# Kernel optimization log

Hardware: AMD Instinct MI355X
Metric: run time of the kernel (lower is better)

## Reference

```python
import jax, jax.numpy as jnp
import numpy as np

DIM = 1024
NUM_HEADS = 16
HEAD_DIM = DIM // NUM_HEADS
SCALE = HEAD_DIM ** -0.5
B, N = 2, 2048


def setup_inputs() -> dict:
    key = jax.random.key(0)
    k_x, k_qkv, k_prjw, k_prjb = jax.random.split(key, 4)
    # nn.Linear(dim, 3*dim, bias=False): weight [3*dim, dim]
    s = 1.0 / np.sqrt(DIM)
    return {
        "x": jax.random.normal(k_x, (B, N, DIM), dtype=jnp.float32),
        "w_qkv": jax.random.uniform(k_qkv, (3 * DIM, DIM), jnp.float32, -s, s),
        "w_prj": jax.random.uniform(k_prjw, (DIM, DIM), jnp.float32, -s, s),
        "b_prj": jax.random.uniform(k_prjb, (DIM,), jnp.float32, -s, s),
    }


def reference(x, w_qkv, w_prj, b_prj):
    Bb, Nn, C = x.shape
    qkv = jnp.einsum("bnc,dc->bnd", x, w_qkv)            # [B,N,3C]
    qkv = qkv.reshape(Bb, Nn, 3, NUM_HEADS, HEAD_DIM)
    qkv = jnp.transpose(qkv, (2, 0, 3, 1, 4))            # [3,B,H,N,hd]
    q, k, v = qkv[0], qkv[1], qkv[2]
    attn = jnp.einsum("bhqd,bhkd->bhqk", q, k) * SCALE   # [B,H,N,N]
    attn = jax.nn.softmax(attn, axis=-1)
    out = jnp.einsum("bhqk,bhkd->bhqd", attn, v)         # [B,H,N,hd]
    out = jnp.transpose(out, (0, 2, 1, 3)).reshape(Bb, Nn, C)
    # dropout layers are identity at eval / p=0
    return jnp.einsum("bnc,dc->bnd", out, w_prj) + b_prj
```

## Files before the change

kernel.cpp:

```cpp
#include <hip/hip_runtime.h>

typedef unsigned short u16;
typedef unsigned int u32;
typedef __attribute__((ext_vector_type(8))) short s16x8;
typedef __attribute__((ext_vector_type(4))) float f32x4;

#define DIM    1024
#define NHEADS 16
#define HD     64
#define NSEQ   2048
#define QKVN   3072

__device__ __forceinline__ u16 f2bf(float f) {
  u32 u = __float_as_uint(f);
  u += 0x7FFF + ((u >> 16) & 1);
  return (u16)(u >> 16);
}

__device__ __forceinline__ float vexp2(float x) {
  float r;
  asm volatile("v_exp_f32 %0, %1" : "=v"(r) : "v"(x));
  return r;
}

__device__ __forceinline__ void async16(const u16* g, u16* l) {
  __builtin_amdgcn_global_load_lds(
      (const __attribute__((address_space(1))) unsigned int*)g,
      (__attribute__((address_space(3))) unsigned int*)l, 16, 0, 0);
}

__global__ void cast_all(const float* __restrict__ x, const float* __restrict__ wq,
                         const float* __restrict__ wp, u16* __restrict__ xo,
                         u16* __restrict__ wqo, u16* __restrict__ wpo) {
  int i = blockIdx.x * 256 + threadIdx.x;
  const float4* src; u16* dst; int off;
  if (i < 1048576)      { src = (const float4*)x;  dst = xo;  off = i; }
  else if (i < 1835008) { src = (const float4*)wq; dst = wqo; off = i - 1048576; }
  else                  { src = (const float4*)wp; dst = wpo; off = i - 1835008; }
  float4 f = src[off];
  ushort4 o;
  o.x = f2bf(f.x); o.y = f2bf(f.y); o.z = f2bf(f.z); o.w = f2bf(f.w);
  ((ushort4*)dst)[off] = o;
}

template <bool FINAL>
__global__ __launch_bounds__(256, 3) void gemm_bt(
    const u16* __restrict__ A, const u16* __restrict__ Bw, u16* __restrict__ qkv,
    u16* __restrict__ vt, const float* __restrict__ bias, float* __restrict__ outp) {
  constexpr int K = 1024;
  constexpr int BM = FINAL ? 64 : 128;
  constexpr int MT = FINAL ? 64 : 32;
  constexpr int IT = FINAL ? 2 : 4;
  constexpr int ACALLS = BM / 8;
  constexpr int TCALLS = ACALLS + 16;
  constexpr int PW = TCALLS / 4;
  const int bm = blockIdx.x % MT;
  const int bn = blockIdx.x / MT;
  const int tid = threadIdx.x;
  const int wave = tid >> 6, lane = tid & 63;
  const int q4 = lane >> 4, l15 = lane & 15;
  const int wm = wave >> 1, wn = wave & 1;
  const int m0 = bm * BM, n0 = bn * 128;

  __shared__ alignas(16) u16 lsA[BM * 64];
  __shared__ alignas(16) u16 lsB[128 * 64];

  f32x4 acc[IT][4];
#pragma unroll
  for (int i = 0; i < IT; i++)
#pragma unroll
    for (int j = 0; j < 4; j++) acc[i][j] = (f32x4){0.f, 0.f, 0.f, 0.f};

  for (int k0 = 0; k0 < K; k0 += 64) {
    __syncthreads();
#pragma unroll
    for (int j = 0; j < PW; ++j) {
      int t = wave * PW + j;
      if (t < ACALLS) {
        int lin = t * 64 + lane;
        int r = lin >> 3, cs = lin & 7, c = cs ^ (r & 7);
        async16(A + (size_t)(m0 + r) * K + k0 + c * 8, lsA + t * 512);
      } else {
        int tb = t - ACALLS;
        int lin = tb * 64 + lane;
        int r = lin >> 3, cs = lin & 7, c = cs ^ (r & 7);
        async16(Bw + (size_t)(n0 + r) * K + k0 + c * 8, lsB + tb * 512);
      }
    }
    __syncthreads();
#pragma unroll
    for (int kc = 0; kc < 2; ++kc) {
      s16x8 af[IT], bfr[4];
#pragma unroll
      for (int i = 0; i < IT; ++i) {
        int r = wm * (IT * 16) + i * 16 + l15;
        int c = (kc * 4 + q4) ^ (r & 7);
        af[i] = *(const s16x8*)(lsA + r * 64 + c * 8);
      }
#pragma unroll
      for (int j = 0; j < 4; ++j) {
        int r = wn * 64 + j * 16 + l15;
        int c = (kc * 4 + q4) ^ (r & 7);
        bfr[j] = *(const s16x8*)(lsB + r * 64 + c * 8);
      }
#pragma unroll
      for (int i = 0; i < IT; ++i)
#pragma unroll
        for (int j = 0; j < 4; ++j)
          acc[i][j] = __builtin_amdgcn_mfma_f32_16x16x32_bf16(af[i], bfr[j], acc[i][j], 0, 0, 0);
    }
  }

#pragma unroll
  for (int i = 0; i < IT; i++) {
#pragma unroll
    for (int j = 0; j < 4; j++) {
      int n = n0 + wn * 64 + j * 16 + l15;
      int mb = m0 + wm * (IT * 16) + i * 16 + q4 * 4;
      if (FINAL) {
#pragma unroll
        for (int r = 0; r < 4; r++)
          outp[(size_t)(mb + r) * DIM + n] = acc[i][j][r] + bias[n];
      } else if (n < 2048) {
#pragma unroll
        for (int r = 0; r < 4; r++)
          qkv[(size_t)(mb + r) * QKVN + n] = f2bf(acc[i][j][r]);
      } else {
        int b = mb >> 11, tok = mb & 2047;
        int h = (n >> 6) & 15, hd = n & 63;
        ushort4 pk;
        pk.x = f2bf(acc[i][j][0]); pk.y = f2bf(acc[i][j][1]);
        pk.z = f2bf(acc[i][j][2]); pk.w = f2bf(acc[i][j][3]);
        *(ushort4*)(vt + ((size_t)((b * NHEADS + h) * HD + hd)) * NSEQ + tok) = pk;
      }
    }
  }
}

__global__ __launch_bounds__(256, 2) void attn_kernel(const u16* __restrict__ qkv,
                                                      const u16* __restrict__ vt,
                                                      u16* __restrict__ aout) {
  const int blk = blockIdx.x;
  const int bh = blk & 31, qt = blk >> 5;
  const int b = bh >> 4, h = bh & 15;
  const int tid = threadIdx.x;
  const int wave = tid >> 6, lane = tid & 63;
  const int q4 = lane >> 4, l15 = lane & 15;

  __shared__ alignas(16) u16 lsK[2][64 * 64];
  __shared__ alignas(16) u16 lsV[2][64 * 64];
  __shared__ alignas(16) u16 lsP[4][16 * 72];

  const float QSCALE = 0.18033688011112042f;
  s16x8 aq[2][2];
#pragma unroll
  for (int rt = 0; rt < 2; ++rt)
#pragma unroll
    for (int kc = 0; kc < 2; ++kc) {
      int row = b * NSEQ + qt * 128 + wave * 32 + rt * 16 + l15;
      uint4 d = *(const uint4*)(qkv + (size_t)row * QKVN + h * HD + kc * 32 + q4 * 8);
      u32 w[4] = {d.x, d.y, d.z, d.w};
      s16x8 f;
#pragma unroll
      for (int j = 0; j < 8; ++j) {
        u16 u = (u16)(w[j >> 1] >> ((j & 1) * 16));
        float v = __uint_as_float(((u32)u) << 16) * QSCALE;
        f[j] = (short)f2bf(v);
      }
      aq[rt][kc] = f;
    }

  f32x4 o[2][4];
  float lsum[2][4] = {{0.f, 0.f, 0.f, 0.f}, {0.f, 0.f, 0.f, 0.f}};
#pragma unroll
  for (int rt = 0; rt < 2; ++rt)
#pragma unroll
    for (int ht = 0; ht < 4; ++ht) o[rt][ht] = (f32x4){0.f, 0.f, 0.f, 0.f};

  auto stage = [&](int kt, int buf) {
#pragma unroll
    for (int j = 0; j < 2; ++j) {
      int t = wave * 2 + j;
      int lin = t * 64 + lane;
      int r = lin >> 3, c = (lin & 7) ^ (r & 7);
      async16(qkv + (size_t)(b * NSEQ + kt * 64 + r) * QKVN + DIM + h * HD + c * 8,
              lsK[buf] + t * 512);
      async16(vt + (size_t)(bh * HD + r) * NSEQ + kt * 64 + c * 8,
              lsV[buf] + t * 512);
    }
  };

  stage(0, 0);

  for (int kt = 0; kt < 32; ++kt) {
    const int buf = kt & 1;
    __syncthreads();
    if (kt + 1 < 32) stage(kt + 1, buf ^ 1);

#pragma unroll
    for (int rt = 0; rt < 2; ++rt) {
      f32x4 s[4];
#pragma unroll
      for (int ct = 0; ct < 4; ++ct) s[ct] = (f32x4){0.f, 0.f, 0.f, 0.f};
#pragma unroll
      for (int kc = 0; kc < 2; ++kc) {
#pragma unroll
        for (int ct = 0; ct < 4; ++ct) {
          int r = ct * 16 + l15;
          int c = (kc * 4 + q4) ^ (r & 7);
          s16x8 bk = *(const s16x8*)(lsK[buf] + r * 64 + c * 8);
          s[ct] = __builtin_amdgcn_mfma_f32_16x16x32_bf16(aq[rt][kc], bk, s[ct], 0, 0, 0);
        }
      }

#pragma unroll
      for (int ct = 0; ct < 4; ++ct)
#pragma unroll
        for (int r = 0; r < 4; ++r) {
          u32 u = __float_as_uint(vexp2(s[ct][r]));
          lsum[rt][r] += __uint_as_float(u & 0xffff0000u);
          lsP[wave][(q4 * 4 + r) * 72 + ct * 16 + l15] = (u16)(u >> 16);
        }

#pragma unroll
      for (int kc = 0; kc < 2; ++kc) {
        s16x8 pa = *(const s16x8*)(lsP[wave] + l15 * 72 + kc * 32 + q4 * 8);
#pragma unroll
        for (int ht = 0; ht < 4; ++ht) {
          int r = ht * 16 + l15;
          int c = (kc * 4 + q4) ^ (r & 7);
          s16x8 vb = *(const s16x8*)(lsV[buf] + r * 64 + c * 8);
          o[rt][ht] = __builtin_amdgcn_mfma_f32_16x16x32_bf16(pa, vb, o[rt][ht], 0, 0, 0);
        }
      }
    }
  }

#pragma unroll
  for (int off = 1; off < 16; off <<= 1)
#pragma unroll
    for (int rt = 0; rt < 2; ++rt)
#pragma unroll
      for (int r = 0; r < 4; ++r) lsum[rt][r] += __shfl_xor(lsum[rt][r], off, 64);

#pragma unroll
  for (int rt = 0; rt < 2; ++rt) {
    float inv[4];
#pragma unroll
    for (int r = 0; r < 4; ++r) inv[r] = 1.0f / lsum[rt][r];
#pragma unroll
    for (int ht = 0; ht < 4; ++ht)
#pragma unroll
      for (int r = 0; r < 4; ++r) {
        int n = qt * 128 + wave * 32 + rt * 16 + q4 * 4 + r;
        int col = h * HD + ht * 16 + l15;
        aout[(size_t)(b * NSEQ + n) * DIM + col] = f2bf(o[rt][ht][r] * inv[r]);
      }
  }
}

extern "C" void kernel_launch(void* const* d_in, const int* in_sizes, int n_in,
                              void* d_out, int out_size, void* d_ws, size_t ws_size,
                              hipStream_t stream) {
  const float* x     = (const float*)d_in[0];
  const float* w_qkv = (const float*)d_in[1];
  const float* w_prj = (const float*)d_in[2];
  const float* b_prj = (const float*)d_in[3];
  float* out = (float*)d_out;

  char* ws = (char*)d_ws;
  u16* x_bf    = (u16*)(ws);
  u16* wqkv_bf = (u16*)(ws + (size_t)(8u << 20));
  u16* wprj_bf = (u16*)(ws + (size_t)(14u << 20));
  u16* qkv     = (u16*)(ws + (size_t)(16u << 20));
  u16* vt      = (u16*)(ws + (size_t)(40u << 20));
  u16* aout    = (u16*)(ws + (size_t)(48u << 20));

  cast_all<<<8192, 256, 0, stream>>>(x, w_qkv, w_prj, x_bf, wqkv_bf, wprj_bf);
  gemm_bt<false><<<32 * 24, 256, 0, stream>>>(x_bf, wqkv_bf, qkv, vt, nullptr, nullptr);
  attn_kernel<<<512, 256, 0, stream>>>(qkv, vt, aout);
  gemm_bt<true><<<64 * 8, 256, 0, stream>>>(aout, wprj_bf, nullptr, nullptr, b_prj, out);
}
```

Measured before the change: 189.4 us.

## Keep softmax P in registers via transposed QK^T and shrink GEMM K-tile

New measurement: 188.0 us. No clear change (-0.7%).

```diff
diff --git a/kernel.cpp b/kernel.cpp
--- a/kernel.cpp
+++ b/kernel.cpp
@@ -3,6 +3,7 @@
 typedef unsigned short u16;
 typedef unsigned int u32;
 typedef __attribute__((ext_vector_type(8))) short s16x8;
+typedef __attribute__((ext_vector_type(4))) short s16x4;
 typedef __attribute__((ext_vector_type(4))) float f32x4;
 
 #define DIM    1024
@@ -51,8 +52,8 @@
   constexpr int BM = FINAL ? 64 : 128;
   constexpr int MT = FINAL ? 64 : 32;
   constexpr int IT = FINAL ? 2 : 4;
-  constexpr int ACALLS = BM / 8;
-  constexpr int TCALLS = ACALLS + 16;
+  constexpr int ACALLS = BM / 16;
+  constexpr int TCALLS = ACALLS + 8;
   constexpr int PW = TCALLS / 4;
   const int bm = blockIdx.x % MT;
   const int bn = blockIdx.x / MT;
@@ -62,8 +63,8 @@
   const int wm = wave >> 1, wn = wave & 1;
   const int m0 = bm * BM, n0 = bn * 128;
 
-  __shared__ alignas(16) u16 lsA[BM * 64];
-  __shared__ alignas(16) u16 lsB[128 * 64];
+  __shared__ alignas(16) u16 lsA[BM * 32];
+  __shared__ alignas(16) u16 lsB[128 * 32];
 
   f32x4 acc[IT][4];
 #pragma unroll
@@ -71,44 +72,35 @@
 #pragma unroll
     for (int j = 0; j < 4; j++) acc[i][j] = (f32x4){0.f, 0.f, 0.f, 0.f};
 
-  for (int k0 = 0; k0 < K; k0 += 64) {
+  for (int k0 = 0; k0 < K; k0 += 32) {
     __syncthreads();
 #pragma unroll
     for (int j = 0; j < PW; ++j) {
       int t = wave * PW + j;
       if (t < ACALLS) {
         int lin = t * 64 + lane;
-        int r = lin >> 3, cs = lin & 7, c = cs ^ (r & 7);
+        int r = lin >> 2, c = lin & 3;
         async16(A + (size_t)(m0 + r) * K + k0 + c * 8, lsA + t * 512);
       } else {
         int tb = t - ACALLS;
         int lin = tb * 64 + lane;
-        int r = lin >> 3, cs = lin & 7, c = cs ^ (r & 7);
+        int r = lin >> 2, c = lin & 3;
         async16(Bw + (size_t)(n0 + r) * K + k0 + c * 8, lsB + tb * 512);
       }
     }
     __syncthreads();
-#pragma unroll
-    for (int kc = 0; kc < 2; ++kc) {
-      s16x8 af[IT], bfr[4];
-#pragma unroll
-      for (int i = 0; i < IT; ++i) {
-        int r = wm * (IT * 16) + i * 16 + l15;
-        int c = (kc * 4 + q4) ^ (r & 7);
-        af[i] = *(const s16x8*)(lsA + r * 64 + c * 8);
-      }
-#pragma unroll
-      for (int j = 0; j < 4; ++j) {
-        int r = wn * 64 + j * 16 + l15;
-        int c = (kc * 4 + q4) ^ (r & 7);
-        bfr[j] = *(const s16x8*)(lsB + r * 64 + c * 8);
-      }
-#pragma unroll
-      for (int i = 0; i < IT; ++i)
-#pragma unroll
-        for (int j = 0; j < 4; ++j)
-          acc[i][j] = __builtin_amdgcn_mfma_f32_16x16x32_bf16(af[i], bfr[j], acc[i][j], 0, 0, 0);
-    }
+    s16x8 af[IT], bfr[4];
+#pragma unroll
+    for (int i = 0; i < IT; ++i)
+      af[i] = *(const s16x8*)(lsA + (wm * (IT * 16) + i * 16 + l15) * 32 + q4 * 8);
+#pragma unroll
+    for (int j = 0; j < 4; ++j)
+      bfr[j] = *(const s16x8*)(lsB + (wn * 64 + j * 16 + l15) * 32 + q4 * 8);
+#pragma unroll
+    for (int i = 0; i < IT; ++i)
+#pragma unroll
+      for (int j = 0; j < 4; ++j)
+        acc[i][j] = __builtin_amdgcn_mfma_f32_16x16x32_bf16(af[i], bfr[j], acc[i][j], 0, 0, 0);
   }
 
 #pragma unroll
@@ -149,7 +141,6 @@
 
   __shared__ alignas(16) u16 lsK[2][64 * 64];
   __shared__ alignas(16) u16 lsV[2][64 * 64];
-  __shared__ alignas(16) u16 lsP[4][16 * 72];
 
   const float QSCALE = 0.18033688011112042f;
   s16x8 aq[2][2];
@@ -171,7 +162,7 @@
     }
 
   f32x4 o[2][4];
-  float lsum[2][4] = {{0.f, 0.f, 0.f, 0.f}, {0.f, 0.f, 0.f, 0.f}};
+  float lsum[2] = {0.f, 0.f};
 #pragma unroll
   for (int rt = 0; rt < 2; ++rt)
 #pragma unroll
@@ -197,57 +188,71 @@
     __syncthreads();
     if (kt + 1 < 32) stage(kt + 1, buf ^ 1);
 
+    s16x8 kf[2][4];
+#pragma unroll
+    for (int kc = 0; kc < 2; ++kc)
+#pragma unroll
+      for (int ct = 0; ct < 4; ++ct) {
+        int r = ct * 16 + l15;
+        int c = (kc * 4 + q4) ^ (r & 7);
+        kf[kc][ct] = *(const s16x8*)(lsK[buf] + r * 64 + c * 8);
+      }
+    s16x4 vf[4][4];
+#pragma unroll
+    for (int ct = 0; ct < 4; ++ct)
+#pragma unroll
+      for (int ht = 0; ht < 4; ++ht) {
+        int row = ht * 16 + l15;
+        int g = ct * 2 + (q4 >> 1);
+        int p = g ^ (row & 7);
+        vf[ct][ht] = *(const s16x4*)(lsV[buf] + row * 64 + p * 8 + (q4 & 1) * 4);
+      }
+
 #pragma unroll
     for (int rt = 0; rt < 2; ++rt) {
-      f32x4 s[4];
-#pragma unroll
-      for (int ct = 0; ct < 4; ++ct) s[ct] = (f32x4){0.f, 0.f, 0.f, 0.f};
-#pragma unroll
-      for (int kc = 0; kc < 2; ++kc) {
-#pragma unroll
-        for (int ct = 0; ct < 4; ++ct) {
-          int r = ct * 16 + l15;
-          int c = (kc * 4 + q4) ^ (r & 7);
-          s16x8 bk = *(const s16x8*)(lsK[buf] + r * 64 + c * 8);
-          s[ct] = __builtin_amdgcn_mfma_f32_16x16x32_bf16(aq[rt][kc], bk, s[ct], 0, 0, 0);
-        }
+      f32x4 st[4];
+#pragma unroll
+      for (int ct = 0; ct < 4; ++ct) st[ct] = (f32x4){0.f, 0.f, 0.f, 0.f};
+#pragma unroll
+      for (int kc = 0; kc < 2; ++kc)
+#pragma unroll
+        for (int ct = 0; ct < 4; ++ct)
+          st[ct] = __builtin_amdgcn_mfma_f32_16x16x32_bf16(kf[kc][ct], aq[rt][kc], st[ct], 0, 0, 0);
+
+      s16x4 pa[4];
+#pragma unroll
+      for (int ct = 0; ct < 4; ++ct) {
+        u32 u0 = __float_as_uint(vexp2(st[ct][0]));
+        u32 u1 = __float_as_uint(vexp2(st[ct][1]));
+        u32 u2 = __float_as_uint(vexp2(st[ct][2]));
+        u32 u3 = __float_as_uint(vexp2(st[ct][3]));
+        lsum[rt] += __uint_as_float(u0 & 0xffff0000u) + __uint_as_float(u1 & 0xffff0000u) +
+                    __uint_as_float(u2 & 0xffff0000u) + __uint_as_float(u3 & 0xffff0000u);
+        union { u32 w[2]; s16x4 v; } pk;
+        pk.w[0] = (u0 >> 16) | (u1 & 0xffff0000u);
+        pk.w[1] = (u2 >> 16) | (u3 & 0xffff0000u);
+        pa[ct] = pk.v;
       }
 
 #pragma unroll
       for (int ct = 0; ct < 4; ++ct)
 #pragma unroll
-        for (int r = 0; r < 4; ++r) {
-          u32 u = __float_as_uint(vexp2(s[ct][r]));
-          lsum[rt][r] += __uint_as_float(u & 0xffff0000u);
-          lsP[wave][(q4 * 4 + r) * 72 + ct * 16 + l15] = (u16)(u >> 16);
-        }
-
-#pragma unroll
-      for (int kc = 0; kc < 2; ++kc) {
-        s16x8 pa = *(const s16x8*)(lsP[wave] + l15 * 72 + kc * 32 + q4 * 8);
-#pragma unroll
-        for (int ht = 0; ht < 4; ++ht) {
-          int r = ht * 16 + l15;
-          int c = (kc * 4 + q4) ^ (r & 7);
-          s16x8 vb = *(const s16x8*)(lsV[buf] + r * 64 + c * 8);
-          o[rt][ht] = __builtin_amdgcn_mfma_f32_16x16x32_bf16(pa, vb, o[rt][ht], 0, 0, 0);
-        }
-      }
-    }
-  }
-
-#pragma unroll
-  for (int off = 1; off < 16; off <<= 1)
-#pragma unroll
-    for (int rt = 0; rt < 2; ++rt)
-#pragma unroll
-      for (int r = 0; r < 4; ++r) lsum[rt][r] += __shfl_xor(lsum[rt][r], off, 64);
+        for (int ht = 0; ht < 4; ++ht)
+          o[rt][ht] = __builtin_amdgcn_mfma_f32_16x16x16bf16_1k(pa[ct], vf[ct][ht], o[rt][ht], 0, 0, 0);
+    }
+  }
+
+#pragma unroll
+  for (int rt = 0; rt < 2; ++rt) {
+    lsum[rt] += __shfl_xor(lsum[rt], 16, 64);
+    lsum[rt] += __shfl_xor(lsum[rt], 32, 64);
+  }
 
 #pragma unroll
   for (int rt = 0; rt < 2; ++rt) {
     float inv[4];
 #pragma unroll
-    for (int r = 0; r < 4; ++r) inv[r] = 1.0f / lsum[rt][r];
+    for (int r = 0; r < 4; ++r) inv[r] = 1.0f / __shfl(lsum[rt], q4 * 4 + r, 64);
 #pragma unroll
     for (int ht = 0; ht < 4; ++ht)
 #pragma unroll
```
